# Performance work log

Hardware: AMD Instinct MI355X
Metric: run time of the kernel (lower is better)

## Reference

```python
import jax, jax.numpy as jnp
import numpy as np

EMB_DIM = 1024
NUM_HEADS = 16
HEAD_DIM = EMB_DIM // NUM_HEADS
SEQ_LEN = 2048
BATCH = 2


def setup_inputs() -> dict:
    key = jax.random.key(0)
    k1, k2, k3 = jax.random.split(key, 3)
    scale = 1.0 / np.sqrt(EMB_DIM)
    x = jax.random.normal(k1, (BATCH, SEQ_LEN, EMB_DIM), dtype=jnp.float32)
    w_qkv = jax.random.normal(k2, (EMB_DIM, 3 * EMB_DIM), dtype=jnp.float32) * scale
    w_proj = jax.random.normal(k3, (EMB_DIM, EMB_DIM), dtype=jnp.float32) * scale
    b_proj = jnp.zeros((EMB_DIM,), dtype=jnp.float32)
    return {"x": x, "w_qkv": w_qkv, "w_proj": w_proj, "b_proj": b_proj}


def reference(x, w_qkv, w_proj, b_proj):
    B, T, E = x.shape
    qkv = x @ w_qkv                                   # [B, T, 3E]
    q, k, v = jnp.split(qkv, 3, axis=-1)
    # -> [B, H, T, D]
    def heads(t):
        return t.reshape(B, T, NUM_HEADS, HEAD_DIM).transpose(0, 2, 1, 3)
    q, k, v = heads(q), heads(k), heads(v)
    att = jnp.einsum("bhqd,bhkd->bhqk", q, k) / np.sqrt(HEAD_DIM).astype(x.dtype)
    causal = jnp.tril(jnp.ones((T, T), dtype=bool))   # True = keep
    att = jnp.where(causal, att, jnp.array(-jnp.inf, dtype=att.dtype))
    att = jax.nn.softmax(att, axis=-1)
    out = jnp.einsum("bhqk,bhkd->bhqd", att, v)       # [B, H, T, D]
    out = out.transpose(0, 2, 1, 3).reshape(B, T, E)
    return out @ w_proj + b_proj
```

## Files before the change

### kernel.cpp

```cpp
#include <hip/hip_runtime.h>

typedef __bf16 bf16x8 __attribute__((ext_vector_type(8)));
typedef __bf16 bf16x4 __attribute__((ext_vector_type(4)));
typedef float  f32x4  __attribute__((ext_vector_type(4)));
typedef float  f32x16 __attribute__((ext_vector_type(16)));
typedef unsigned u32x2 __attribute__((ext_vector_type(2)));
typedef unsigned u32x4 __attribute__((ext_vector_type(4)));

#define T_SEQ 2048
#define NH    16
#define HD    64
#define EMB   1024
#define BATCH 2
#define QSCALE 0.18033688f

__device__ __forceinline__ void gload_lds16(const void* g, void* lds) {
  __builtin_amdgcn_global_load_lds(
      (__attribute__((address_space(1))) void*)(g),
      (__attribute__((address_space(3))) void*)(lds), 16, 0, 0);
}

__device__ __forceinline__ f32x16 mfma32(bf16x8 a, bf16x8 b, f32x16 c) {
  return __builtin_amdgcn_mfma_f32_32x32x16_bf16(a, b, c, 0, 0, 0);
}

__device__ __forceinline__ unsigned cvtpk(float lo, float hi) {
  unsigned short a = __builtin_bit_cast(unsigned short, (__bf16)lo);
  unsigned short b = __builtin_bit_cast(unsigned short, (__bf16)hi);
  return (unsigned)a | ((unsigned)b << 16);
}

__global__ __launch_bounds__(256) void cvt_bf16(const float* __restrict__ in,
                                                __bf16* __restrict__ out, int n) {
  int i = (blockIdx.x * 256 + threadIdx.x) * 8;
  if (i >= n) return;
  f32x4 a = *(const f32x4*)(in + i);
  f32x4 b = *(const f32x4*)(in + i + 4);
  bf16x8 v;
  v[0] = (__bf16)a[0]; v[1] = (__bf16)a[1]; v[2] = (__bf16)a[2]; v[3] = (__bf16)a[3];
  v[4] = (__bf16)b[0]; v[5] = (__bf16)b[1]; v[6] = (__bf16)b[2]; v[7] = (__bf16)b[3];
  *(bf16x8*)(out + i) = v;
}

__global__ __launch_bounds__(256) void transpose_cvt(const float* __restrict__ in,
                                                     __bf16* __restrict__ out,
                                                     int rows, int cols) {
  __shared__ float tile[32][33];
  int c0 = blockIdx.x * 32, r0 = blockIdx.y * 32;
  int tx = threadIdx.x & 31, ty = threadIdx.x >> 5;
#pragma unroll
  for (int j = 0; j < 32; j += 8)
    tile[ty + j][tx] = in[(size_t)(r0 + ty + j) * cols + c0 + tx];
  __syncthreads();
#pragma unroll
  for (int j = 0; j < 32; j += 8)
    out[(size_t)(c0 + ty + j) * rows + r0 + tx] = (__bf16)tile[tx][ty + j];
}

template <int MODE>
__global__ __launch_bounds__(256) void gemm_bt(
    const __bf16* __restrict__ A, const __bf16* __restrict__ Bt, int K,
    __bf16* __restrict__ Qo, __bf16* __restrict__ Ko, __bf16* __restrict__ Vt,
    const float* __restrict__ bias, float* __restrict__ Cout) {
  __shared__ alignas(16) __bf16 sA[2][128 * 32];
  __shared__ alignas(16) __bf16 sB[2][128 * 32];
  const int tid = threadIdx.x;
  const int w = tid >> 6, l = tid & 63;
  const int m0 = blockIdx.y * 128, n0 = blockIdx.x * 128;
  const int lc = l & 15, lu = l >> 4;
  const int mw = (w >> 1) * 64, nw = (w & 1) * 64;
  const int rA = l >> 2;
  const int usw = (((l & 3) ^ ((rA >> 1) & 3))) * 8;
  const int rsw = (lu ^ ((lc >> 1) & 3)) * 8;

  f32x4 acc[4][4] = {};

  auto stage = [&](int buf, int kt) {
#pragma unroll
    for (int i = 0; i < 2; ++i) {
      int rr = (w * 2 + i) * 16;
      gload_lds16(A  + (size_t)(m0 + rr + rA) * K + kt + usw, &sA[buf][rr * 32]);
      gload_lds16(Bt + (size_t)(n0 + rr + rA) * K + kt + usw, &sB[buf][rr * 32]);
    }
  };

  stage(0, 0);
  asm volatile("s_waitcnt vmcnt(0)" ::: "memory");
  __syncthreads();

  int buf = 0;
  for (int kt = 0; kt < K; kt += 32) {
    if (kt + 32 < K) stage(buf ^ 1, kt + 32);

    bf16x8 af[4], bfr[4];
#pragma unroll
    for (int f = 0; f < 4; ++f) {
      af[f]  = *(const bf16x8*)(&sA[buf][(mw + f * 16 + lc) * 32 + rsw]);
      bfr[f] = *(const bf16x8*)(&sB[buf][(nw + f * 16 + lc) * 32 + rsw]);
    }
#pragma unroll
    for (int mf = 0; mf < 4; ++mf)
#pragma unroll
      for (int nf = 0; nf < 4; ++nf)
        acc[mf][nf] = __builtin_amdgcn_mfma_f32_16x16x32_bf16(af[mf], bfr[nf],
                                                              acc[mf][nf], 0, 0, 0);
    asm volatile("s_waitcnt vmcnt(0)" ::: "memory");
    __syncthreads();
    buf ^= 1;
  }

#pragma unroll
  for (int mf = 0; mf < 4; ++mf) {
#pragma unroll
    for (int nf = 0; nf < 4; ++nf) {
#pragma unroll
      for (int r = 0; r < 4; ++r) {
        int mg = m0 + mw + mf * 16 + lu * 4 + r;
        int ng = n0 + nw + nf * 16 + lc;
        float v = acc[mf][nf][r];
        if (MODE == 0) {
          int part = ng >> 10;
          int h = (ng >> 6) & 15;
          int d = ng & 63;
          int b = mg >> 11;
          int t = mg & 2047;
          if (part == 0) {
            Qo[(((size_t)(b * NH + h)) * T_SEQ + t) * HD + d] = (__bf16)(v * QSCALE);
          } else if (part == 1) {
            Ko[(((size_t)(b * NH + h)) * T_SEQ + t) * HD + d] = (__bf16)v;
          } else {
            Vt[(((size_t)(b * NH + h)) * HD + d) * T_SEQ + t] = (__bf16)v;
          }
        } else {
          Cout[(size_t)mg * EMB + ng] = v + bias[ng];
        }
      }
    }
  }
}

__device__ __forceinline__ bf16x8 lfrag(const __bf16* b, int row, int u) {
  return *(const bf16x8*)(b + row * 64 + ((u ^ (row & 7)) << 3));
}

__device__ __forceinline__ void cmask(f32x16& s0, f32x16& s1, int k0, int hi, int q) {
#pragma unroll
  for (int r = 0; r < 16; ++r) {
    int kk = k0 + 4 * hi + (r & 3) + 8 * (r >> 2);
    if (kk > q) s0[r] = -1e30f;
    if (kk + 32 > q) s1[r] = -1e30f;
  }
}

__device__ __forceinline__ void softmax_pack(
    f32x16& s0, f32x16& s1, f32x16& o0, f32x16& o1,
    float& m, float& ls, u32x4 (&pf)[4]) {
  float mx[16];
#pragma unroll
  for (int r = 0; r < 16; ++r) mx[r] = fmaxf(s0[r], s1[r]);
#pragma unroll
  for (int st = 8; st > 0; st >>= 1)
#pragma unroll
    for (int r = 0; r < 16; ++r) if (r < st) mx[r] = fmaxf(mx[r], mx[r + st]);
  float pmax = fmaxf(mx[0], __shfl_xor(mx[0], 32));
  if (!__all(pmax <= m + 8.0f)) {
    float mn = fmaxf(m, pmax);
    float al = __builtin_amdgcn_exp2f(m - mn);
    m = mn;
    ls *= al;
#pragma unroll
    for (int r = 0; r < 16; ++r) { o0[r] *= al; o1[r] *= al; }
  }
  float ps = 0.f;
  f32x16 p0, p1;
#pragma unroll
  for (int r = 0; r < 16; ++r) {
    p0[r] = __builtin_amdgcn_exp2f(s0[r] - m); ps += p0[r];
    p1[r] = __builtin_amdgcn_exp2f(s1[r] - m); ps += p1[r];
  }
  ps += __shfl_xor(ps, 32);
  ls += ps;
#pragma unroll
  for (int kt = 0; kt < 2; ++kt) {
    const f32x16& p = kt ? p1 : p0;
#pragma unroll
    for (int kh = 0; kh < 2; ++kh) {
      unsigned c01 = cvtpk(p[kh * 8 + 0], p[kh * 8 + 1]);
      unsigned c23 = cvtpk(p[kh * 8 + 2], p[kh * 8 + 3]);
      unsigned c45 = cvtpk(p[kh * 8 + 4], p[kh * 8 + 5]);
      unsigned c67 = cvtpk(p[kh * 8 + 6], p[kh * 8 + 7]);
      u32x2 a = __builtin_amdgcn_permlane32_swap(c01, c45, false, false);
      u32x2 c = __builtin_amdgcn_permlane32_swap(c23, c67, false, false);
      u32x4 r; r[0] = a[0]; r[1] = c[0]; r[2] = a[1]; r[3] = c[1];
      pf[kt * 2 + kh] = r;
    }
  }
}

__device__ __forceinline__ void dump_state(float* mo, float* mm, int reg, int l,
                                           const f32x16& o0, const f32x16& o1,
                                           float m, float ls) {
  float* po = mo + reg * 2048 + l;
#pragma unroll
  for (int r = 0; r < 16; ++r) { po[r * 64] = o0[r]; po[(16 + r) * 64] = o1[r]; }
  mm[reg * 128 + l] = m;
  mm[reg * 128 + 64 + l] = ls;
}

__device__ __forceinline__ void merge_write(const float* mo, const float* mm,
                                            int reg, int l, int hi,
                                            const f32x16& o0, const f32x16& o1,
                                            float m, float ls,
                                            __bf16* O, size_t rowbase) {
  float m1 = mm[reg * 128 + l];
  float l1 = mm[reg * 128 + 64 + l];
  float mn = fmaxf(m, m1);
  float a0 = __builtin_amdgcn_exp2f(m - mn);
  float a1 = __builtin_amdgcn_exp2f(m1 - mn);
  float inv = 1.f / (ls * a0 + l1 * a1);
  const float* po = mo + reg * 2048 + l;
#pragma unroll
  for (int dt = 0; dt < 2; ++dt) {
    const f32x16& ov = dt ? o1 : o0;
#pragma unroll
    for (int rg = 0; rg < 4; ++rg) {
      bf16x4 vv;
#pragma unroll
      for (int j = 0; j < 4; ++j) {
        int r = rg * 4 + j;
        float oth = po[(dt * 16 + r) * 64];
        vv[j] = (__bf16)((ov[r] * a0 + oth * a1) * inv);
      }
      int d = dt * 32 + rg * 8 + 4 * hi;
      *(bf16x4*)(O + rowbase + d) = vv;
    }
  }
}

__global__ __launch_bounds__(256, 2) void attn(
    const __bf16* __restrict__ Q,
    const __bf16* __restrict__ K,
    const __bf16* __restrict__ Vt,
    __bf16* __restrict__ O) {
  __shared__ alignas(16) __bf16 sKV[8][64 * 64];
  __shared__ alignas(16) float mls[4 * 2 * 64];

  const int x = blockIdx.x, bh = blockIdx.y;
  const int tid = threadIdx.x, w = tid >> 6, l = tid & 63;
  const int lq = l & 31, hi = l >> 5;
  const int gc = w & 1;
  const int s  = w >> 1;

  const __bf16* Qh = Q + (size_t)bh * T_SEQ * HD;
  const __bf16* Kh = K + (size_t)bh * T_SEQ * HD;
  const __bf16* Vh = Vt + (size_t)bh * HD * T_SEQ;

  const int qL = x * 64 + s * 32;
  const int qH = (31 - x) * 64 + s * 32;
  const int nt = 32 - x;
  const int nsup = (nt + 1) >> 1;

  bf16x8 qfL[4], qfH[4];
#pragma unroll
  for (int dc = 0; dc < 4; ++dc) {
    qfL[dc] = *(const bf16x8*)(Qh + (size_t)(qL + lq) * HD + dc * 16 + hi * 8);
    qfH[dc] = *(const bf16x8*)(Qh + (size_t)(qH + lq) * HD + dc * 16 + hi * 8);
  }

  f32x16 oL0 = {}, oL1 = {}, oH0 = {}, oH1 = {};
  float mL = -1e30f, lsL = 0.f, mH = -1e30f, lsH = 0.f;

  const int r8 = l >> 3;
  const int uswE = ((l & 7) ^ r8) << 3;

  auto stage = [&](int buf, int ss) {
    int t = 2 * ss + gc;
    if (t > 31) t = 31;
    int k0s = t * 64;
    __bf16* dst = &sKV[s * 4 + buf * 2 + gc][0];
    if (s == 0) {
#pragma unroll
      for (int i = 0; i < 8; ++i)
        gload_lds16(Kh + (size_t)(k0s + i * 8 + r8) * HD + uswE, dst + i * 512);
    } else {
#pragma unroll
      for (int i = 0; i < 8; ++i)
        gload_lds16(Vh + (size_t)(i * 8 + r8) * T_SEQ + k0s + uswE, dst + i * 512);
    }
  };

  stage(0, 0);
  asm volatile("s_waitcnt vmcnt(0)" ::: "memory");
  __syncthreads();

  int buf = 0;
  for (int ss = 0; ss < nsup; ++ss) {
    if (ss + 1 < nsup) stage(buf ^ 1, ss + 1);
    const int tg = 2 * ss + gc;
    const bool doH = (tg < nt);
    const bool doL = (tg <= x);
    if (doH) {
      const __bf16* sKb = &sKV[buf * 2 + gc][0];
      const __bf16* sVb = &sKV[4 + buf * 2 + gc][0];
      f32x16 sH0 = {}, sH1 = {}, sL0 = {}, sL1 = {};
#pragma unroll
      for (int dc = 0; dc < 4; ++dc) {
        bf16x8 kf0 = lfrag(sKb, lq, dc * 2 + hi);
        bf16x8 kf1 = lfrag(sKb, 32 + lq, dc * 2 + hi);
        sH0 = mfma32(kf0, qfH[dc], sH0);
        sH1 = mfma32(kf1, qfH[dc], sH1);
        if (doL) {
          sL0 = mfma32(kf0, qfL[dc], sL0);
          sL1 = mfma32(kf1, qfL[dc], sL1);
        }
      }
      const int k0 = tg * 64;
      if (tg == nt - 1) cmask(sH0, sH1, k0, hi, qH + lq);
      u32x4 pfH[4], pfL[4];
      softmax_pack(sH0, sH1, oH0, oH1, mH, lsH, pfH);
      if (doL) {
        if (tg == x) cmask(sL0, sL1, k0, hi, qL + lq);
        softmax_pack(sL0, sL1, oL0, oL1, mL, lsL, pfL);
      }
#pragma unroll
      for (int ks = 0; ks < 4; ++ks) {
        bf16x8 vf0 = lfrag(sVb, lq, ks * 2 + hi);
        bf16x8 vf1 = lfrag(sVb, 32 + lq, ks * 2 + hi);
        bf16x8 pH = __builtin_bit_cast(bf16x8, pfH[ks]);
        oH0 = mfma32(vf0, pH, oH0);
        oH1 = mfma32(vf1, pH, oH1);
        if (doL) {
          bf16x8 pL = __builtin_bit_cast(bf16x8, pfL[ks]);
          oL0 = mfma32(vf0, pL, oL0);
          oL1 = mfma32(vf1, pL, oL1);
        }
      }
    }
    asm volatile("s_waitcnt vmcnt(0)" ::: "memory");
    __syncthreads();
    buf ^= 1;
  }

  float* mo = (float*)&sKV[0][0];
  if (gc == 1) {
    dump_state(mo, mls, s * 2 + 0, l, oH0, oH1, mH, lsH);
    dump_state(mo, mls, s * 2 + 1, l, oL0, oL1, mL, lsL);
  }
  __syncthreads();
  if (gc == 0) {
    const int b = bh >> 4, h = bh & 15;
    size_t rowH = (size_t)(b * T_SEQ + qH + lq) * EMB + h * HD;
    size_t rowL = (size_t)(b * T_SEQ + qL + lq) * EMB + h * HD;
    merge_write(mo, mls, s * 2 + 0, l, hi, oH0, oH1, mH, lsH, O, rowH);
    merge_write(mo, mls, s * 2 + 1, l, hi, oL0, oL1, mL, lsL, O, rowL);
  }
}

extern "C" void kernel_launch(void* const* d_in, const int* in_sizes, int n_in,
                              void* d_out, int out_size, void* d_ws, size_t ws_size,
                              hipStream_t stream) {
  const float* x      = (const float*)d_in[0];
  const float* w_qkv  = (const float*)d_in[1];
  const float* w_proj = (const float*)d_in[2];
  const float* b_proj = (const float*)d_in[3];
  float* out = (float*)d_out;

  char* ws = (char*)d_ws;
  __bf16* xb     = (__bf16*)(ws);
  __bf16* wqkvT  = (__bf16*)(ws + (8u  << 20));
  __bf16* wprojT = (__bf16*)(ws + (14u << 20));
  __bf16* Qw     = (__bf16*)(ws + (16u << 20));
  __bf16* Kw     = (__bf16*)(ws + (24u << 20));
  __bf16* Vw     = (__bf16*)(ws + (32u << 20));
  __bf16* Ow     = xb;

  cvt_bf16<<<2048, 256, 0, stream>>>(x, xb, 4096 * 1024);
  transpose_cvt<<<dim3(3072 / 32, 1024 / 32), 256, 0, stream>>>(w_qkv, wqkvT, 1024, 3072);
  transpose_cvt<<<dim3(1024 / 32, 1024 / 32), 256, 0, stream>>>(w_proj, wprojT, 1024, 1024);

  gemm_bt<0><<<dim3(3072 / 128, 4096 / 128), 256, 0, stream>>>(
      xb, wqkvT, 1024, Qw, Kw, Vw, nullptr, nullptr);

  attn<<<dim3(16, BATCH * NH), 256, 0, stream>>>(Qw, Kw, Vw, Ow);

  gemm_bt<1><<<dim3(1024 / 128, 4096 / 128), 256, 0, stream>>>(
      Ow, wprojT, 1024, nullptr, nullptr, nullptr, b_proj, out);
}
```

Before: 124.8 us.

## Replace QKV GEMM with 256x256 tiled, 8-wave ping-pong pipelined kernel

Splits the generic GEMM into a dedicated QKV projection kernel that uses 256x256 block tiles, 512 threads, a BK of 64 and an XOR-swizzled LDS layout. The K loop is broken into four quarter-phases that interleave LDS fragment reads, async global-to-LDS staging and MFMA bursts, with barriers and s_setprio controlling the order. The goal is better data reuse per tile and overlap of memory traffic with matrix math in the largest GEMM. In exchange it uses 128KB of LDS per block and launches only 192 blocks, which may leave CUs underused, and the barrier-heavy schedule is fragile.

```diff
diff --git a/kernel.cpp b/kernel.cpp
--- a/kernel.cpp
+++ b/kernel.cpp
@@ -22,6 +22,10 @@
 
 __device__ __forceinline__ f32x16 mfma32(bf16x8 a, bf16x8 b, f32x16 c) {
   return __builtin_amdgcn_mfma_f32_32x32x16_bf16(a, b, c, 0, 0, 0);
+}
+
+__device__ __forceinline__ f32x4 mfma16(bf16x8 a, bf16x8 b, f32x4 c) {
+  return __builtin_amdgcn_mfma_f32_16x16x32_bf16(a, b, c, 0, 0, 0);
 }
 
 __device__ __forceinline__ unsigned cvtpk(float lo, float hi) {
@@ -57,10 +61,161 @@
     out[(size_t)(c0 + ty + j) * rows + r0 + tx] = (__bf16)tile[tx][ty + j];
 }
 
-template <int MODE>
-__global__ __launch_bounds__(256) void gemm_bt(
+__global__ __launch_bounds__(512, 2) void gemm_qkv(
+    const __bf16* __restrict__ A, const __bf16* __restrict__ Bt,
+    __bf16* __restrict__ Qo, __bf16* __restrict__ Ko, __bf16* __restrict__ Vt) {
+  constexpr int K = 1024, NT = K / 64;
+  __shared__ alignas(16) __bf16 sA[2][256 * 64];
+  __shared__ alignas(16) __bf16 sB[2][256 * 64];
+  const int tid = threadIdx.x;
+  const int w = tid >> 6, l = tid & 63;
+  const int wr = w >> 2, wc = w & 3;
+  const int lc = l & 15, lu = l >> 4;
+  const int m0 = blockIdx.y * 256, n0 = blockIdx.x * 256;
+
+  const int srow = tid >> 3;
+  const int gsw = ((tid & 7) ^ (srow & 7)) * 8;
+
+  f32x4 acc[8][4] = {};
+
+  auto stageA = [&](int buf, int t, int h) {
+    const __bf16* src = A + (size_t)(m0 + h * 128) * K + t * 64 + gsw;
+    __bf16* dst = &sA[buf][(h * 128 + w * 8) * 64];
+#pragma unroll
+    for (int j = 0; j < 2; ++j)
+      gload_lds16(src + (size_t)(j * 64 + srow) * K, dst + j * 64 * 64);
+  };
+  auto stageB = [&](int buf, int t, int h) {
+    const __bf16* src = Bt + (size_t)(n0 + h * 128) * K + t * 64 + gsw;
+    __bf16* dst = &sB[buf][(h * 128 + w * 8) * 64];
+#pragma unroll
+    for (int j = 0; j < 2; ++j)
+      gload_lds16(src + (size_t)(j * 64 + srow) * K, dst + j * 64 * 64);
+  };
+
+  auto rdA = [&](int buf, int m, int kk) -> bf16x8 {
+    int row = wr * 128 + m * 16 + lc;
+    return *(const bf16x8*)(&sA[buf][row * 64 + (((kk << 2) + lu) ^ (lc & 7)) * 8]);
+  };
+  auto rdB = [&](int buf, int n, int kk) -> bf16x8 {
+    int row = wc * 64 + n * 16 + lc;
+    return *(const bf16x8*)(&sB[buf][row * 64 + (((kk << 2) + lu) ^ (lc & 7)) * 8]);
+  };
+
+  stageA(0, 0, 0); stageA(0, 0, 1);
+  stageB(0, 0, 0); stageB(0, 0, 1);
+  stageA(1, 1, 0); stageA(1, 1, 1);
+  asm volatile("s_waitcnt vmcnt(4)" ::: "memory");
+  __builtin_amdgcn_s_barrier();
+  __builtin_amdgcn_sched_barrier(0);
+
+#pragma unroll 2
+  for (int t = 0; t < NT; ++t) {
+    const int cb = t & 1;
+    bf16x8 af0[4][2], af1[4][2], b0[2][2], b1[2][2];
+
+#pragma unroll
+    for (int m = 0; m < 4; ++m) { af0[m][0] = rdA(cb, m, 0); af0[m][1] = rdA(cb, m, 1); }
+#pragma unroll
+    for (int n = 0; n < 2; ++n) { b0[n][0] = rdB(cb, n, 0); b0[n][1] = rdB(cb, n, 1); }
+    if (t + 1 < NT) stageB(cb ^ 1, t + 1, 0);
+    __builtin_amdgcn_s_barrier();
+    asm volatile("s_waitcnt lgkmcnt(0)" ::: "memory");
+    __builtin_amdgcn_sched_barrier(0);
+    __builtin_amdgcn_s_setprio(1);
+#pragma unroll
+    for (int m = 0; m < 4; ++m)
+#pragma unroll
+      for (int n = 0; n < 2; ++n) {
+        acc[m][n] = mfma16(af0[m][0], b0[n][0], acc[m][n]);
+        acc[m][n] = mfma16(af0[m][1], b0[n][1], acc[m][n]);
+      }
+    __builtin_amdgcn_s_setprio(0);
+    __builtin_amdgcn_s_barrier();
+    __builtin_amdgcn_sched_barrier(0);
+
+#pragma unroll
+    for (int m = 0; m < 4; ++m) { af1[m][0] = rdA(cb, 4 + m, 0); af1[m][1] = rdA(cb, 4 + m, 1); }
+    if (t + 1 < NT) stageB(cb ^ 1, t + 1, 1);
+    __builtin_amdgcn_s_barrier();
+    asm volatile("s_waitcnt lgkmcnt(0)" ::: "memory");
+    __builtin_amdgcn_sched_barrier(0);
+    __builtin_amdgcn_s_setprio(1);
+#pragma unroll
+    for (int m = 0; m < 4; ++m)
+#pragma unroll
+      for (int n = 0; n < 2; ++n) {
+        acc[4 + m][n] = mfma16(af1[m][0], b0[n][0], acc[4 + m][n]);
+        acc[4 + m][n] = mfma16(af1[m][1], b0[n][1], acc[4 + m][n]);
+      }
+    __builtin_amdgcn_s_setprio(0);
+    __builtin_amdgcn_s_barrier();
+    __builtin_amdgcn_sched_barrier(0);
+
+#pragma unroll
+    for (int n = 0; n < 2; ++n) { b1[n][0] = rdB(cb, 2 + n, 0); b1[n][1] = rdB(cb, 2 + n, 1); }
+    if (t + 2 < NT) stageA(cb, t + 2, 0);
+    __builtin_amdgcn_s_barrier();
+    asm volatile("s_waitcnt lgkmcnt(0)" ::: "memory");
+    __builtin_amdgcn_sched_barrier(0);
+    __builtin_amdgcn_s_setprio(1);
+#pragma unroll
+    for (int m = 0; m < 4; ++m)
+#pragma unroll
+      for (int n = 0; n < 2; ++n) {
+        acc[4 + m][2 + n] = mfma16(af1[m][0], b1[n][0], acc[4 + m][2 + n]);
+        acc[4 + m][2 + n] = mfma16(af1[m][1], b1[n][1], acc[4 + m][2 + n]);
+      }
+    __builtin_amdgcn_s_setprio(0);
+    __builtin_amdgcn_s_barrier();
+    __builtin_amdgcn_sched_barrier(0);
+
+    if (t + 2 < NT) stageA(cb, t + 2, 1);
+    __builtin_amdgcn_s_barrier();
+    __builtin_amdgcn_sched_barrier(0);
+    __builtin_amdgcn_s_setprio(1);
+#pragma unroll
+    for (int m = 0; m < 4; ++m)
+#pragma unroll
+      for (int n = 0; n < 2; ++n) {
+        acc[m][2 + n] = mfma16(af0[m][0], b1[n][0], acc[m][2 + n]);
+        acc[m][2 + n] = mfma16(af0[m][1], b1[n][1], acc[m][2 + n]);
+      }
+    __builtin_amdgcn_s_setprio(0);
+    if (t + 2 < NT) { asm volatile("s_waitcnt vmcnt(4)" ::: "memory"); }
+    else            { asm volatile("s_waitcnt vmcnt(0)" ::: "memory"); }
+    __builtin_amdgcn_s_barrier();
+    __builtin_amdgcn_sched_barrier(0);
+  }
+
+#pragma unroll
+  for (int mf = 0; mf < 8; ++mf) {
+#pragma unroll
+    for (int nf = 0; nf < 4; ++nf) {
+#pragma unroll
+      for (int r = 0; r < 4; ++r) {
+        int mg = m0 + wr * 128 + mf * 16 + lu * 4 + r;
+        int ng = n0 + wc * 64 + nf * 16 + lc;
+        float v = acc[mf][nf][r];
+        int part = ng >> 10;
+        int h = (ng >> 6) & 15;
+        int d = ng & 63;
+        int b = mg >> 11;
+        int tq = mg & 2047;
+        if (part == 0) {
+          Qo[(((size_t)(b * NH + h)) * T_SEQ + tq) * HD + d] = (__bf16)(v * QSCALE);
+        } else if (part == 1) {
+          Ko[(((size_t)(b * NH + h)) * T_SEQ + tq) * HD + d] = (__bf16)v;
+        } else {
+          Vt[(((size_t)(b * NH + h)) * HD + d) * T_SEQ + tq] = (__bf16)v;
+        }
+      }
+    }
+  }
+}
+
+__global__ __launch_bounds__(256) void gemm_proj(
     const __bf16* __restrict__ A, const __bf16* __restrict__ Bt, int K,
-    __bf16* __restrict__ Qo, __bf16* __restrict__ Ko, __bf16* __restrict__ Vt,
     const float* __restrict__ bias, float* __restrict__ Cout) {
   __shared__ alignas(16) __bf16 sA[2][128 * 32];
   __shared__ alignas(16) __bf16 sB[2][128 * 32];
@@ -91,7 +246,6 @@
   int buf = 0;
   for (int kt = 0; kt < K; kt += 32) {
     if (kt + 32 < K) stage(buf ^ 1, kt + 32);
-
     bf16x8 af[4], bfr[4];
 #pragma unroll
     for (int f = 0; f < 4; ++f) {
@@ -102,41 +256,22 @@
     for (int mf = 0; mf < 4; ++mf)
 #pragma unroll
       for (int nf = 0; nf < 4; ++nf)
-        acc[mf][nf] = __builtin_amdgcn_mfma_f32_16x16x32_bf16(af[mf], bfr[nf],
-                                                              acc[mf][nf], 0, 0, 0);
+        acc[mf][nf] = mfma16(af[mf], bfr[nf], acc[mf][nf]);
     asm volatile("s_waitcnt vmcnt(0)" ::: "memory");
     __syncthreads();
     buf ^= 1;
   }
 
 #pragma unroll
-  for (int mf = 0; mf < 4; ++mf) {
-#pragma unroll
-    for (int nf = 0; nf < 4; ++nf) {
+  for (int mf = 0; mf < 4; ++mf)
+#pragma unroll
+    for (int nf = 0; nf < 4; ++nf)
 #pragma unroll
       for (int r = 0; r < 4; ++r) {
         int mg = m0 + mw + mf * 16 + lu * 4 + r;
         int ng = n0 + nw + nf * 16 + lc;
-        float v = acc[mf][nf][r];
-        if (MODE == 0) {
-          int part = ng >> 10;
-          int h = (ng >> 6) & 15;
-          int d = ng & 63;
-          int b = mg >> 11;
-          int t = mg & 2047;
-          if (part == 0) {
-            Qo[(((size_t)(b * NH + h)) * T_SEQ + t) * HD + d] = (__bf16)(v * QSCALE);
-          } else if (part == 1) {
-            Ko[(((size_t)(b * NH + h)) * T_SEQ + t) * HD + d] = (__bf16)v;
-          } else {
-            Vt[(((size_t)(b * NH + h)) * HD + d) * T_SEQ + t] = (__bf16)v;
-          }
-        } else {
-          Cout[(size_t)mg * EMB + ng] = v + bias[ng];
-        }
-      }
-    }
-  }
+        Cout[(size_t)mg * EMB + ng] = acc[mf][nf][r] + bias[ng];
+      }
 }
 
 __device__ __forceinline__ bf16x8 lfrag(const __bf16* b, int row, int u) {
@@ -378,11 +513,11 @@
   transpose_cvt<<<dim3(3072 / 32, 1024 / 32), 256, 0, stream>>>(w_qkv, wqkvT, 1024, 3072);
   transpose_cvt<<<dim3(1024 / 32, 1024 / 32), 256, 0, stream>>>(w_proj, wprojT, 1024, 1024);
 
-  gemm_bt<0><<<dim3(3072 / 128, 4096 / 128), 256, 0, stream>>>(
-      xb, wqkvT, 1024, Qw, Kw, Vw, nullptr, nullptr);
+  gemm_qkv<<<dim3(3072 / 256, 4096 / 256), 512, 0, stream>>>(
+      xb, wqkvT, Qw, Kw, Vw);
 
   attn<<<dim3(16, BATCH * NH), 256, 0, stream>>>(Qw, Kw, Vw, Ow);
 
-  gemm_bt<1><<<dim3(1024 / 128, 4096 / 128), 256, 0, stream>>>(
-      Ow, wprojT, 1024, nullptr, nullptr, nullptr, b_proj, out);
-}
+  gemm_proj<<<dim3(1024 / 128, 4096 / 128), 256, 0, stream>>>(
+      Ow, wprojT, 1024, b_proj, out);
+}
```

Result: slower. 146.0 us (+16.9%).

## Shrink attention KV tiles to 32 keys and raise occupancy to four blocks

Applied to the files above, without the earlier changes.

The attention kernel now stages 32-key K/V tiles instead of 64-key tiles, halving LDS per block, and computes one 32x32 score tile per wave per step with per-32-key causal diagonal masking. Launch bounds move from 2 to 4 blocks per CU to exploit the smaller LDS footprint and register use. The intent is finer causal granularity, so less masked work is done, and more latency hiding through occupancy. In exchange there are twice as many loop iterations and barriers, and less MFMA work per synchronisation.

```diff
diff --git a/kernel.cpp b/kernel.cpp
--- a/kernel.cpp
+++ b/kernel.cpp
@@ -22,6 +22,10 @@
 
 __device__ __forceinline__ f32x16 mfma32(bf16x8 a, bf16x8 b, f32x16 c) {
   return __builtin_amdgcn_mfma_f32_32x32x16_bf16(a, b, c, 0, 0, 0);
+}
+
+__device__ __forceinline__ f32x4 mfma16(bf16x8 a, bf16x8 b, f32x4 c) {
+  return __builtin_amdgcn_mfma_f32_16x16x32_bf16(a, b, c, 0, 0, 0);
 }
 
 __device__ __forceinline__ unsigned cvtpk(float lo, float hi) {
@@ -91,7 +95,6 @@
   int buf = 0;
   for (int kt = 0; kt < K; kt += 32) {
     if (kt + 32 < K) stage(buf ^ 1, kt + 32);
-
     bf16x8 af[4], bfr[4];
 #pragma unroll
     for (int f = 0; f < 4; ++f) {
@@ -102,8 +105,7 @@
     for (int mf = 0; mf < 4; ++mf)
 #pragma unroll
       for (int nf = 0; nf < 4; ++nf)
-        acc[mf][nf] = __builtin_amdgcn_mfma_f32_16x16x32_bf16(af[mf], bfr[nf],
-                                                              acc[mf][nf], 0, 0, 0);
+        acc[mf][nf] = mfma16(af[mf], bfr[nf], acc[mf][nf]);
     asm volatile("s_waitcnt vmcnt(0)" ::: "memory");
     __syncthreads();
     buf ^= 1;
@@ -139,29 +141,24 @@
   }
 }
 
-__device__ __forceinline__ bf16x8 lfrag(const __bf16* b, int row, int u) {
-  return *(const bf16x8*)(b + row * 64 + ((u ^ (row & 7)) << 3));
-}
-
-__device__ __forceinline__ void cmask(f32x16& s0, f32x16& s1, int k0, int hi, int q) {
+__device__ __forceinline__ void cmask32(f32x16& s0, int k0, int hi, int q) {
 #pragma unroll
   for (int r = 0; r < 16; ++r) {
     int kk = k0 + 4 * hi + (r & 3) + 8 * (r >> 2);
     if (kk > q) s0[r] = -1e30f;
-    if (kk + 32 > q) s1[r] = -1e30f;
-  }
-}
-
-__device__ __forceinline__ void softmax_pack(
-    f32x16& s0, f32x16& s1, f32x16& o0, f32x16& o1,
-    float& m, float& ls, u32x4 (&pf)[4]) {
-  float mx[16];
-#pragma unroll
-  for (int r = 0; r < 16; ++r) mx[r] = fmaxf(s0[r], s1[r]);
-#pragma unroll
-  for (int st = 8; st > 0; st >>= 1)
-#pragma unroll
-    for (int r = 0; r < 16; ++r) if (r < st) mx[r] = fmaxf(mx[r], mx[r + st]);
+  }
+}
+
+__device__ __forceinline__ void softmax_pack32(
+    f32x16& s0, f32x16& o0, f32x16& o1,
+    float& m, float& ls, u32x4 (&pf)[2]) {
+  float mx[8];
+#pragma unroll
+  for (int r = 0; r < 8; ++r) mx[r] = fmaxf(s0[r], s0[r + 8]);
+#pragma unroll
+  for (int st = 4; st > 0; st >>= 1)
+#pragma unroll
+    for (int r = 0; r < 8; ++r) if (r < st) mx[r] = fmaxf(mx[r], mx[r + st]);
   float pmax = fmaxf(mx[0], __shfl_xor(mx[0], 32));
   if (!__all(pmax <= m + 8.0f)) {
     float mn = fmaxf(m, pmax);
@@ -172,28 +169,21 @@
     for (int r = 0; r < 16; ++r) { o0[r] *= al; o1[r] *= al; }
   }
   float ps = 0.f;
-  f32x16 p0, p1;
-#pragma unroll
-  for (int r = 0; r < 16; ++r) {
-    p0[r] = __builtin_amdgcn_exp2f(s0[r] - m); ps += p0[r];
-    p1[r] = __builtin_amdgcn_exp2f(s1[r] - m); ps += p1[r];
-  }
+  f32x16 p;
+#pragma unroll
+  for (int r = 0; r < 16; ++r) { p[r] = __builtin_amdgcn_exp2f(s0[r] - m); ps += p[r]; }
   ps += __shfl_xor(ps, 32);
   ls += ps;
 #pragma unroll
-  for (int kt = 0; kt < 2; ++kt) {
-    const f32x16& p = kt ? p1 : p0;
-#pragma unroll
-    for (int kh = 0; kh < 2; ++kh) {
-      unsigned c01 = cvtpk(p[kh * 8 + 0], p[kh * 8 + 1]);
-      unsigned c23 = cvtpk(p[kh * 8 + 2], p[kh * 8 + 3]);
-      unsigned c45 = cvtpk(p[kh * 8 + 4], p[kh * 8 + 5]);
-      unsigned c67 = cvtpk(p[kh * 8 + 6], p[kh * 8 + 7]);
-      u32x2 a = __builtin_amdgcn_permlane32_swap(c01, c45, false, false);
-      u32x2 c = __builtin_amdgcn_permlane32_swap(c23, c67, false, false);
-      u32x4 r; r[0] = a[0]; r[1] = c[0]; r[2] = a[1]; r[3] = c[1];
-      pf[kt * 2 + kh] = r;
-    }
+  for (int kh = 0; kh < 2; ++kh) {
+    unsigned c01 = cvtpk(p[kh * 8 + 0], p[kh * 8 + 1]);
+    unsigned c23 = cvtpk(p[kh * 8 + 2], p[kh * 8 + 3]);
+    unsigned c45 = cvtpk(p[kh * 8 + 4], p[kh * 8 + 5]);
+    unsigned c67 = cvtpk(p[kh * 8 + 6], p[kh * 8 + 7]);
+    u32x2 a = __builtin_amdgcn_permlane32_swap(c01, c45, false, false);
+    u32x2 c = __builtin_amdgcn_permlane32_swap(c23, c67, false, false);
+    u32x4 r; r[0] = a[0]; r[1] = c[0]; r[2] = a[1]; r[3] = c[1];
+    pf[kh] = r;
   }
 }
 
@@ -237,12 +227,12 @@
   }
 }
 
-__global__ __launch_bounds__(256, 2) void attn(
+__global__ __launch_bounds__(256, 4) void attn(
     const __bf16* __restrict__ Q,
     const __bf16* __restrict__ K,
     const __bf16* __restrict__ Vt,
     __bf16* __restrict__ O) {
-  __shared__ alignas(16) __bf16 sKV[8][64 * 64];
+  __shared__ alignas(16) __bf16 sKV[8][32 * 64];
   __shared__ alignas(16) float mls[4 * 2 * 64];
 
   const int x = blockIdx.x, bh = blockIdx.y;
@@ -257,8 +247,9 @@
 
   const int qL = x * 64 + s * 32;
   const int qH = (31 - x) * 64 + s * 32;
-  const int nt = 32 - x;
-  const int nsup = (nt + 1) >> 1;
+  const int nsup = 32 - x;
+  const int diagH = 2 * (31 - x) + s;
+  const int diagL = 2 * x + s;
 
   bf16x8 qfL[4], qfH[4];
 #pragma unroll
@@ -270,23 +261,31 @@
   f32x16 oL0 = {}, oL1 = {}, oH0 = {}, oH1 = {};
   float mL = -1e30f, lsL = 0.f, mH = -1e30f, lsH = 0.f;
 
-  const int r8 = l >> 3;
-  const int uswE = ((l & 7) ^ r8) << 3;
+  const int r8k = l >> 3;
+  const int kswz = ((l & 7) ^ (r8k & 7)) * 8;
+  const int r4v = l >> 2;
+  const int vswz = ((l & 3) ^ (r4v & 3)) * 8;
 
   auto stage = [&](int buf, int ss) {
     int t = 2 * ss + gc;
-    if (t > 31) t = 31;
-    int k0s = t * 64;
+    int k0s = t * 32;
     __bf16* dst = &sKV[s * 4 + buf * 2 + gc][0];
     if (s == 0) {
 #pragma unroll
-      for (int i = 0; i < 8; ++i)
-        gload_lds16(Kh + (size_t)(k0s + i * 8 + r8) * HD + uswE, dst + i * 512);
+      for (int i = 0; i < 4; ++i)
+        gload_lds16(Kh + (size_t)(k0s + i * 8 + r8k) * HD + kswz, dst + i * 512);
     } else {
 #pragma unroll
-      for (int i = 0; i < 8; ++i)
-        gload_lds16(Vh + (size_t)(i * 8 + r8) * T_SEQ + k0s + uswE, dst + i * 512);
-    }
+      for (int i = 0; i < 4; ++i)
+        gload_lds16(Vh + (size_t)(i * 16 + r4v) * T_SEQ + k0s + vswz, dst + i * 512);
+    }
+  };
+
+  auto kfrag = [&](const __bf16* b, int row, int u) -> bf16x8 {
+    return *(const bf16x8*)(b + row * 64 + ((u ^ (row & 7)) << 3));
+  };
+  auto vfrag = [&](const __bf16* b, int row, int u) -> bf16x8 {
+    return *(const bf16x8*)(b + row * 32 + ((u ^ (row & 3)) << 3));
   };
 
   stage(0, 0);
@@ -297,35 +296,30 @@
   for (int ss = 0; ss < nsup; ++ss) {
     if (ss + 1 < nsup) stage(buf ^ 1, ss + 1);
     const int tg = 2 * ss + gc;
-    const bool doH = (tg < nt);
-    const bool doL = (tg <= x);
+    const bool doH = (tg <= diagH);
+    const bool doL = (tg <= diagL);
     if (doH) {
       const __bf16* sKb = &sKV[buf * 2 + gc][0];
       const __bf16* sVb = &sKV[4 + buf * 2 + gc][0];
-      f32x16 sH0 = {}, sH1 = {}, sL0 = {}, sL1 = {};
+      f32x16 sH = {}, sL = {};
 #pragma unroll
       for (int dc = 0; dc < 4; ++dc) {
-        bf16x8 kf0 = lfrag(sKb, lq, dc * 2 + hi);
-        bf16x8 kf1 = lfrag(sKb, 32 + lq, dc * 2 + hi);
-        sH0 = mfma32(kf0, qfH[dc], sH0);
-        sH1 = mfma32(kf1, qfH[dc], sH1);
-        if (doL) {
-          sL0 = mfma32(kf0, qfL[dc], sL0);
-          sL1 = mfma32(kf1, qfL[dc], sL1);
-        }
-      }
-      const int k0 = tg * 64;
-      if (tg == nt - 1) cmask(sH0, sH1, k0, hi, qH + lq);
-      u32x4 pfH[4], pfL[4];
-      softmax_pack(sH0, sH1, oH0, oH1, mH, lsH, pfH);
+        bf16x8 kf = kfrag(sKb, lq, dc * 2 + hi);
+        sH = mfma32(kf, qfH[dc], sH);
+        if (doL) sL = mfma32(kf, qfL[dc], sL);
+      }
+      const int k0 = tg * 32;
+      if (tg == diagH) cmask32(sH, k0, hi, qH + lq);
+      u32x4 pfH[2], pfL[2];
+      softmax_pack32(sH, oH0, oH1, mH, lsH, pfH);
       if (doL) {
-        if (tg == x) cmask(sL0, sL1, k0, hi, qL + lq);
-        softmax_pack(sL0, sL1, oL0, oL1, mL, lsL, pfL);
-      }
-#pragma unroll
-      for (int ks = 0; ks < 4; ++ks) {
-        bf16x8 vf0 = lfrag(sVb, lq, ks * 2 + hi);
-        bf16x8 vf1 = lfrag(sVb, 32 + lq, ks * 2 + hi);
+        if (tg == diagL) cmask32(sL, k0, hi, qL + lq);
+        softmax_pack32(sL, oL0, oL1, mL, lsL, pfL);
+      }
+#pragma unroll
+      for (int ks = 0; ks < 2; ++ks) {
+        bf16x8 vf0 = vfrag(sVb, lq, ks * 2 + hi);
+        bf16x8 vf1 = vfrag(sVb, 32 + lq, ks * 2 + hi);
         bf16x8 pH = __builtin_bit_cast(bf16x8, pfH[ks]);
         oH0 = mfma32(vf0, pH, oH0);
         oH1 = mfma32(vf1, pH, oH1);
```

New measurement: 230.4 us. 1.85x slower.
